# Optimization experiments

Hardware: AMD Instinct MI355X
Metric: run time of the kernel (lower is better)

## Reference

```python
import jax, jax.numpy as jnp
import numpy as np

OFFSET = 8.0
COLLISION_THRESHOLD = 0.0


def _safe_norm(d):
    # L2 norm over last axis with zero (not NaN) gradient at 0, matching torch.norm backward.
    s = jnp.sum(d * d, axis=-1)
    return jnp.where(s == 0, 0.0, jnp.sqrt(jnp.where(s == 0, 1.0, s)))


def setup_inputs() -> dict:
    key = jax.random.key(0)
    ks = jax.random.split(key, 8)
    A, M, T, O = 256, 16, 80, 64
    return {
        "targets": jax.random.normal(ks[0], (A, T, 2), jnp.float32) * 10.0,
        "target_mask": jax.random.randint(ks[1], (A, T), 0, 2, jnp.int32),
        "traj_preds": jax.random.normal(ks[2], (A, M, T, 4), jnp.float32) * 10.0,
        "mode_probs": jax.random.uniform(ks[3], (A, M), jnp.float32),
        "agent_fut_width": jax.random.uniform(ks[4], (A, T), jnp.float32) * 2.0,
        "other_fut_trajs": jax.random.normal(ks[5], (A, O, T, 2), jnp.float32) * 10.0,
        "other_fut_masks": jax.random.randint(ks[6], (A, O, T), 0, 2, jnp.int32),
        "other_fut_widths": jax.random.uniform(ks[7], (A, O, T), jnp.float32) * 2.0,
    }


def reference(targets, target_mask, traj_preds, mode_probs, agent_fut_width,
              other_fut_trajs, other_fut_masks, other_fut_widths):
    tm = target_mask.astype(jnp.float32)                 # [A, T]
    tm_e = tm[:, None, :]                                # [A, 1, T] broadcasts over modes

    preds = traj_preds * tm_e[..., None]                 # [A, M, T, 4]
    tgt = targets[:, None, :, :] * tm_e[..., None]       # [A, M(broadcast), T, 2]

    l2 = _safe_norm(preds[..., :2] - tgt)                # [A, M, T]
    total_l2 = l2.sum(axis=-1)                           # [A, M]

    # Pairwise collision check against other agents' trajectories.
    pi = preds[..., :2]                                  # [A, M, T, 2]
    diff = pi[:, :, None, :, :] - other_fut_trajs[:, None, :, :, :]  # [A, M, O, T, 2]
    dist = jnp.sqrt(jnp.sum(diff * diff, axis=-1))       # [A, M, O, T]

    w_i = agent_fut_width[:, None, None, :]              # [A, 1, 1, T]
    w_o = other_fut_widths[:, None, :, :]                # [A, 1, O, T]
    radius = 0.5 * (w_i + w_o) + COLLISION_THRESHOLD

    valid = (tm_e[:, :, None, :] > 0) & (other_fut_masks[:, None, :, :] > 0)  # [A, M(b), O, T]
    collide = (dist <= radius) & valid                   # [A, M, O, T]
    collision_matrix = jnp.any(collide, axis=2).astype(jnp.float32)  # [A, M, T]
    collision = collision_matrix.sum(axis=-1)            # [A, M]

    l2_penalty = -(total_l2 - OFFSET)
    collision_penalty = -collision * 100.0
    total = l2_penalty + collision_penalty
    return total, collision_penalty, l2_penalty
```

## Files before the change

### kernel.cpp

```cpp
#include <hip/hip_runtime.h>
#include <hip/hip_bf16.h>


#define T_DIM 80
#define M_DIM 16
#define O_DIM 64
#define TH 40

__global__ __launch_bounds__(256) void prc_kernel(
    const float* __restrict__ targets,
    const int*   __restrict__ tmask,
    const float* __restrict__ preds,
    const float* __restrict__ afw,
    const float* __restrict__ otraj,
    const int*   __restrict__ omask,
    const float* __restrict__ owid,
    float* __restrict__ out, int A)
{
    const int a = blockIdx.x;
    const int tid = threadIdx.x;

    __shared__ float  tmS[T_DIM];
    __shared__ float  wiS[T_DIM];
    __shared__ float2 tgS[T_DIM];
    __shared__ float2 piS[T_DIM][M_DIM + 1];
    __shared__ float  oxS[O_DIM][TH + 1];
    __shared__ float  oyS[O_DIM][TH + 1];
    __shared__ float  raS[O_DIM][TH + 1];
    __shared__ float  l2S[4][M_DIM];
    __shared__ int    cnS[4][M_DIM];

    const float2* tg2 = (const float2*)targets;
    const float4* pr4 = (const float4*)preds;
    const float2* ot2 = (const float2*)otraj;

    if (tid < T_DIM) {
        int t = tid;
        float tm = (float)tmask[a * T_DIM + t];
        tmS[t] = tm;
        wiS[t] = afw[a * T_DIM + t];
        float2 g = tg2[a * T_DIM + t];
        tgS[t] = make_float2(__fmul_rn(g.x, tm), __fmul_rn(g.y, tm));
    }
    __syncthreads();

    #pragma unroll
    for (int k = 0; k < 5; ++k) {
        int i = tid + k * 256;
        int m = i / T_DIM;
        int t = i - m * T_DIM;
        float4 p = pr4[a * (M_DIM * T_DIM) + i];
        float tm = tmS[t];
        piS[t][m] = make_float2(__fmul_rn(p.x, tm), __fmul_rn(p.y, tm));
    }
    __syncthreads();

    if (tid < 64) {
        int m = tid & 15, tc4 = tid >> 4;
        float acc = 0.0f;
        for (int tt = 0; tt < 20; ++tt) {
            int t = tc4 * 20 + tt;
            float2 p = piS[t][m];
            float2 g = tgS[t];
            float dx = __fsub_rn(p.x, g.x);
            float dy = __fsub_rn(p.y, g.y);
            float s  = __fadd_rn(__fmul_rn(dx, dx), __fmul_rn(dy, dy));
            acc = __fadd_rn(acc, __fsqrt_rn(s));
        }
        l2S[tc4][m] = acc;
    }

    const int o  = tid & 63;
    const int tc = tid >> 6;
    int ctr = 0;

    for (int h = 0; h < 2; ++h) {
        __syncthreads();
        #pragma unroll
        for (int k = 0; k < 10; ++k) {
            int j  = tid + k * 256;
            int oo = j / TH;
            int tl = j - oo * TH;
            int t  = h * TH + tl;
            int gi = (a * O_DIM + oo) * T_DIM + t;
            float2 tr = ot2[gi];
            int   om = omask[gi];
            float wo = owid[gi];
            float tm = tmS[t];
            float rad = (tm != 0.0f && om > 0)
                      ? __fmul_rn(0.5f, __fadd_rn(wiS[t], wo))
                      : -1.0f;
            oxS[oo][tl] = tr.x;
            oyS[oo][tl] = tr.y;
            raS[oo][tl] = rad;
        }
        __syncthreads();

        for (int tt = 0; tt < 10; ++tt) {
            int tl = tc * 10 + tt;
            int t  = h * TH + tl;
            if (tmS[t] == 0.0f) continue;
            float ox  = oxS[o][tl];
            float oy  = oyS[o][tl];
            float rad = raS[o][tl];
            unsigned mm = 0;
            #pragma unroll
            for (int m = 0; m < M_DIM; ++m) {
                float2 p = piS[t][m];
                float dx = __fsub_rn(p.x, ox);
                float dy = __fsub_rn(p.y, oy);
                float s  = __fadd_rn(__fmul_rn(dx, dx), __fmul_rn(dy, dy));
                float dist = __fsqrt_rn(s);
                if (dist <= rad) mm |= (1u << m);
            }
            int v = (int)mm;
            v |= __shfl_xor(v, 1, 64);
            v |= __shfl_xor(v, 2, 64);
            v |= __shfl_xor(v, 4, 64);
            v |= __shfl_xor(v, 8, 64);
            v |= __shfl_xor(v, 16, 64);
            v |= __shfl_xor(v, 32, 64);
            ctr += (v >> (tid & 15)) & 1;
        }
    }
    if ((tid & 63) < 16) cnS[tc][tid & 15] = ctr;
    __syncthreads();

    if (tid < M_DIM) {
        int m = tid;
        float tl2 = __fadd_rn(__fadd_rn(__fadd_rn(l2S[0][m], l2S[1][m]),
                                        l2S[2][m]), l2S[3][m]);
        int cnt = cnS[0][m] + cnS[1][m] + cnS[2][m] + cnS[3][m];
        float l2p = __fsub_rn(8.0f, tl2);
        float cp  = __fmul_rn(-100.0f, (float)cnt);
        int AM = A * M_DIM;
        out[a * M_DIM + m]          = __fadd_rn(l2p, cp);
        out[AM + a * M_DIM + m]     = cp;
        out[2 * AM + a * M_DIM + m] = l2p;
    }
}

extern "C" void kernel_launch(void* const* d_in, const int* in_sizes, int n_in,
                              void* d_out, int out_size, void* d_ws, size_t ws_size,
                              hipStream_t stream) {
    const float* targets = (const float*)d_in[0];
    const int*   tmask   = (const int*)  d_in[1];
    const float* preds   = (const float*)d_in[2];
    const float* afw     = (const float*)d_in[4];
    const float* otraj   = (const float*)d_in[5];
    const int*   omask   = (const int*)  d_in[6];
    const float* owid    = (const float*)d_in[7];
    float* out = (float*)d_out;

    int A = in_sizes[1] / T_DIM;

    prc_kernel<<<A, 256, 0, stream>>>(targets, tmask, preds, afw,
                                      otraj, omask, owid, out, A);
}
```

Before: 107.4 us.

## Compare squared distance to precomputed threshold, use ballot, widen blocks to 1024

Replaces the per-pair sqrt with a comparison of squared distance against an exactly rounded squared-radius threshold, computed once per (other, t) in double precision so results stay bit-identical. Collision reduction per mode now uses a wave ballot instead of a six-step shuffle OR chain, with per-wave counters. The block grows to 1024 threads (16 waves), each wave owning timesteps, and the L2 computation is spread over 256 threads. More threads per block raise register pressure and reduce how many blocks can be resident at once.

Measured after the change: 91.09 us. 1.18x faster.

```diff
diff --git a/kernel.cpp b/kernel.cpp
--- a/kernel.cpp
+++ b/kernel.cpp
@@ -1,13 +1,15 @@
 #include <hip/hip_runtime.h>
 #include <hip/hip_bf16.h>
+#include <math.h>
 
 
 #define T_DIM 80
 #define M_DIM 16
 #define O_DIM 64
 #define TH 40
+#define NW 16
 
-__global__ __launch_bounds__(256) void prc_kernel(
+__global__ __launch_bounds__(1024) void prc_kernel(
     const float* __restrict__ targets,
     const int*   __restrict__ tmask,
     const float* __restrict__ preds,
@@ -17,8 +19,10 @@
     const float* __restrict__ owid,
     float* __restrict__ out, int A)
 {
-    const int a = blockIdx.x;
-    const int tid = threadIdx.x;
+    const int a    = blockIdx.x;
+    const int tid  = threadIdx.x;
+    const int lane = tid & 63;
+    const int w    = tid >> 6;
 
     __shared__ float  tmS[T_DIM];
     __shared__ float  wiS[T_DIM];
@@ -26,9 +30,9 @@
     __shared__ float2 piS[T_DIM][M_DIM + 1];
     __shared__ float  oxS[O_DIM][TH + 1];
     __shared__ float  oyS[O_DIM][TH + 1];
-    __shared__ float  raS[O_DIM][TH + 1];
-    __shared__ float  l2S[4][M_DIM];
-    __shared__ int    cnS[4][M_DIM];
+    __shared__ float  r2S[O_DIM][TH + 1];
+    __shared__ float  l2S[16][M_DIM + 1];
+    __shared__ int    cnW[NW][M_DIM];
 
     const float2* tg2 = (const float2*)targets;
     const float4* pr4 = (const float4*)preds;
@@ -45,94 +49,102 @@
     __syncthreads();
 
     #pragma unroll
-    for (int k = 0; k < 5; ++k) {
-        int i = tid + k * 256;
-        int m = i / T_DIM;
-        int t = i - m * T_DIM;
-        float4 p = pr4[a * (M_DIM * T_DIM) + i];
-        float tm = tmS[t];
-        piS[t][m] = make_float2(__fmul_rn(p.x, tm), __fmul_rn(p.y, tm));
-    }
-    __syncthreads();
-
-    if (tid < 64) {
-        int m = tid & 15, tc4 = tid >> 4;
-        float acc = 0.0f;
-        for (int tt = 0; tt < 20; ++tt) {
-            int t = tc4 * 20 + tt;
-            float2 p = piS[t][m];
-            float2 g = tgS[t];
-            float dx = __fsub_rn(p.x, g.x);
-            float dy = __fsub_rn(p.y, g.y);
-            float s  = __fadd_rn(__fmul_rn(dx, dx), __fmul_rn(dy, dy));
-            acc = __fadd_rn(acc, __fsqrt_rn(s));
+    for (int k = 0; k < 2; ++k) {
+        int i = tid + k * 1024;
+        if (i < M_DIM * T_DIM) {
+            int m = i / T_DIM;
+            int t = i - m * T_DIM;
+            float4 p = pr4[a * (M_DIM * T_DIM) + i];
+            float tm = tmS[t];
+            piS[t][m] = make_float2(__fmul_rn(p.x, tm), __fmul_rn(p.y, tm));
         }
-        l2S[tc4][m] = acc;
     }
 
-    const int o  = tid & 63;
-    const int tc = tid >> 6;
-    int ctr = 0;
+    int cnt[M_DIM];
+    #pragma unroll
+    for (int m = 0; m < M_DIM; ++m) cnt[m] = 0;
 
     for (int h = 0; h < 2; ++h) {
-        __syncthreads();
+        if (h) __syncthreads();
         #pragma unroll
-        for (int k = 0; k < 10; ++k) {
-            int j  = tid + k * 256;
-            int oo = j / TH;
-            int tl = j - oo * TH;
-            int t  = h * TH + tl;
-            int gi = (a * O_DIM + oo) * T_DIM + t;
-            float2 tr = ot2[gi];
-            int   om = omask[gi];
-            float wo = owid[gi];
-            float tm = tmS[t];
-            float rad = (tm != 0.0f && om > 0)
-                      ? __fmul_rn(0.5f, __fadd_rn(wiS[t], wo))
-                      : -1.0f;
-            oxS[oo][tl] = tr.x;
-            oyS[oo][tl] = tr.y;
-            raS[oo][tl] = rad;
+        for (int k = 0; k < 3; ++k) {
+            int j = tid + k * 1024;
+            if (j < O_DIM * TH) {
+                int oo = j / TH;
+                int tl = j - oo * TH;
+                int t  = h * TH + tl;
+                int gi = (a * O_DIM + oo) * T_DIM + t;
+                float2 tr = ot2[gi];
+                int   om = omask[gi];
+                float wo = owid[gi];
+                float tm = tmS[t];
+                float r2 = -1.0f;
+                if (tm != 0.0f && om > 0) {
+                    float rad = __fmul_rn(0.5f, __fadd_rn(wiS[t], wo));
+                    float nxt = nextafterf(rad, __builtin_inff());
+                    double thr  = 0.5 * ((double)rad + (double)nxt);
+                    double thr2 = thr * thr;
+                    float f = (float)thr2;
+                    if ((double)f > thr2) f = nextafterf(f, -__builtin_inff());
+                    r2 = f;
+                }
+                oxS[oo][tl] = tr.x;
+                oyS[oo][tl] = tr.y;
+                r2S[oo][tl] = r2;
+            }
         }
         __syncthreads();
 
-        for (int tt = 0; tt < 10; ++tt) {
-            int tl = tc * 10 + tt;
-            int t  = h * TH + tl;
+        if (h == 0 && tid < 256) {
+            int m = tid & 15, tq = tid >> 4;
+            float acc = 0.0f;
+            #pragma unroll
+            for (int tt = 0; tt < 5; ++tt) {
+                int t = tq * 5 + tt;
+                float2 p = piS[t][m];
+                float2 g = tgS[t];
+                float dx = __fsub_rn(p.x, g.x);
+                float dy = __fsub_rn(p.y, g.y);
+                float s  = __fadd_rn(__fmul_rn(dx, dx), __fmul_rn(dy, dy));
+                acc = __fadd_rn(acc, __fsqrt_rn(s));
+            }
+            l2S[tq][m] = acc;
+        }
+
+        for (int tl = w; tl < TH; tl += NW) {
+            int t = h * TH + tl;
             if (tmS[t] == 0.0f) continue;
-            float ox  = oxS[o][tl];
-            float oy  = oyS[o][tl];
-            float rad = raS[o][tl];
-            unsigned mm = 0;
+            float ox = oxS[lane][tl];
+            float oy = oyS[lane][tl];
+            float r2 = r2S[lane][tl];
             #pragma unroll
             for (int m = 0; m < M_DIM; ++m) {
                 float2 p = piS[t][m];
                 float dx = __fsub_rn(p.x, ox);
                 float dy = __fsub_rn(p.y, oy);
                 float s  = __fadd_rn(__fmul_rn(dx, dx), __fmul_rn(dy, dy));
-                float dist = __fsqrt_rn(s);
-                if (dist <= rad) mm |= (1u << m);
+                unsigned long long b = __ballot(s <= r2);
+                cnt[m] += (b != 0ull) ? 1 : 0;
             }
-            int v = (int)mm;
-            v |= __shfl_xor(v, 1, 64);
-            v |= __shfl_xor(v, 2, 64);
-            v |= __shfl_xor(v, 4, 64);
-            v |= __shfl_xor(v, 8, 64);
-            v |= __shfl_xor(v, 16, 64);
-            v |= __shfl_xor(v, 32, 64);
-            ctr += (v >> (tid & 15)) & 1;
         }
     }
-    if ((tid & 63) < 16) cnS[tc][tid & 15] = ctr;
+
+    if (lane == 0) {
+        #pragma unroll
+        for (int m = 0; m < M_DIM; ++m) cnW[w][m] = cnt[m];
+    }
     __syncthreads();
 
     if (tid < M_DIM) {
         int m = tid;
-        float tl2 = __fadd_rn(__fadd_rn(__fadd_rn(l2S[0][m], l2S[1][m]),
-                                        l2S[2][m]), l2S[3][m]);
-        int cnt = cnS[0][m] + cnS[1][m] + cnS[2][m] + cnS[3][m];
+        float tl2 = 0.0f;
+        #pragma unroll
+        for (int j = 0; j < 16; ++j) tl2 = __fadd_rn(tl2, l2S[j][m]);
+        int c = 0;
+        #pragma unroll
+        for (int j = 0; j < NW; ++j) c += cnW[j][m];
         float l2p = __fsub_rn(8.0f, tl2);
-        float cp  = __fmul_rn(-100.0f, (float)cnt);
+        float cp  = __fmul_rn(-100.0f, (float)c);
         int AM = A * M_DIM;
         out[a * M_DIM + m]          = __fadd_rn(l2p, cp);
         out[AM + a * M_DIM + m]     = cp;
@@ -154,6 +166,6 @@
 
     int A = in_sizes[1] / T_DIM;
 
-    prc_kernel<<<A, 256, 0, stream>>>(targets, tmask, preds, afw,
-                                      otraj, omask, owid, out, A);
+    prc_kernel<<<A, 1024, 0, stream>>>(targets, tmask, preds, afw,
+                                       otraj, omask, owid, out, A);
 }
```
